# Kernel tuning notes

Measured on AMD Instinct MI355X. Metric: run time of the kernel, lower is better.

The kernel has to match this reference:

```python
import jax, jax.numpy as jnp
import numpy as np

N = 50000      # nodes
E = 800000     # top-down edges (before self-loops)
IN = 256       # in_dim
HID = 64       # hidden_dim
H = 4          # heads
SLOPE = 0.2    # PyG GATConv leaky_relu negative_slope


def setup_inputs() -> dict:
    key = jax.random.key(0)
    ks = jax.random.split(key, 12)
    g = lambda k, s, fan: jax.random.normal(k, s, dtype=jnp.float32) / np.float32(np.sqrt(fan))
    return {
        "x": jax.random.normal(ks[0], (N, IN), dtype=jnp.float32),
        "root_features": jax.random.normal(ks[1], (N, IN), dtype=jnp.float32),
        "edge_index": jax.random.randint(ks[2], (2, E), 0, N, dtype=jnp.int32),
        "W1": g(ks[3], (H * HID, IN), IN),
        "a_src1": g(ks[4], (H, HID), HID),
        "a_dst1": g(ks[5], (H, HID), HID),
        "b1": jnp.zeros((H * HID,), jnp.float32),
        "W2": g(ks[6], (H * HID, H * HID), H * HID),
        "a_src2": g(ks[7], (H, HID), HID),
        "a_dst2": g(ks[8], (H, HID), HID),
        "b2": jnp.zeros((HID,), jnp.float32),
        "Wr": g(ks[9], (HID, IN), IN),
        "br": jnp.zeros((HID,), jnp.float32),
    }


def gat_conv(h_in, src, dst, W, a_src, a_dst, bias, concat):
    """PyG GATConv (eval mode): gather -> attention logit -> segment softmax -> scatter."""
    h = (h_in @ W.T).reshape(-1, H, HID)                 # [N, H, C]
    alpha_s = jnp.einsum('nhc,hc->nh', h, a_src)         # [N, H]
    alpha_d = jnp.einsum('nhc,hc->nh', h, a_dst)
    logits = jax.nn.leaky_relu(alpha_s[src] + alpha_d[dst], SLOPE)   # [Etot, H]
    # numerically stable softmax over incoming edges of each dst node
    m = jax.ops.segment_max(logits, dst, num_segments=N)             # [N, H]
    e = jnp.exp(logits - m[dst])
    denom = jax.ops.segment_sum(e, dst, num_segments=N)              # [N, H]
    alpha = e / denom[dst]                                           # self-loops => denom > 0
    out = jax.ops.segment_sum(alpha[:, :, None] * h[src], dst, num_segments=N)  # [N, H, C]
    if concat:
        return out.reshape(-1, H * HID) + bias
    return out.mean(axis=1) + bias


def reference(x, root_features, edge_index, W1, a_src1, a_dst1, b1,
              W2, a_src2, a_dst2, b2, Wr, br):
    # PyG GATConv adds self-loops by default
    loops = jnp.arange(N, dtype=edge_index.dtype)
    src = jnp.concatenate([edge_index[0], loops])   # parents (message sources)
    dst = jnp.concatenate([edge_index[1], loops])   # children (aggregation targets)

    h = gat_conv(x, src, dst, W1, a_src1, a_dst1, b1, concat=True)   # [N, H*HID]
    h = jax.nn.relu(h)                                               # dropout = identity in eval
    h = gat_conv(h, src, dst, W2, a_src2, a_dst2, b2, concat=False)  # [N, HID]
    return h + root_features @ Wr.T + br
```

## Files before the change

kernel.cpp:

```cpp
#include <hip/hip_runtime.h>
#include <hip/hip_bf16.h>
#include <math.h>

#define NN   50000
#define EE   800000
#define ETOT (EE + NN)
#define KDIM 256
#define HEADS 4
#define HIDD 64
#define DCAP 64

typedef float  f32x4  __attribute__((ext_vector_type(4)));
typedef short  bf16x8 __attribute__((ext_vector_type(8)));

__device__ __forceinline__ float b2f(unsigned short u) {
    union { float f; unsigned int i; } v; v.i = (unsigned int)u << 16; return v.f;
}
__device__ __forceinline__ unsigned short f2b(float f) {
    union { float f; unsigned int i; } v; v.f = f;
    return (unsigned short)((v.i + 0x7fffu + ((v.i >> 16) & 1u)) >> 16);
}
__device__ __forceinline__ float lrelu(float x) { return x >= 0.f ? x : 0.2f * x; }

#define CASTB 144

__global__ __launch_bounds__(256) void prep_k(
    const float* __restrict__ W1, const float* __restrict__ W2,
    const float* __restrict__ Wr, unsigned short* __restrict__ wout)
{
    int i = (blockIdx.x * 256 + threadIdx.x) * 4;
    const float* src;
    int off;
    if (i < 65536)        { src = W1; off = 0; }
    else if (i < 131072)  { src = W2; off = 65536; }
    else                  { src = Wr; off = 131072; }
    float4 v = *reinterpret_cast<const float4*>(src + (i - off));
    ushort4 o;
    o.x = f2b(v.x); o.y = f2b(v.y); o.z = f2b(v.z); o.w = f2b(v.w);
    *reinterpret_cast<ushort4*>(wout + i) = o;
}

template<bool AF32, int NCT, bool ALPHA, bool OUTF32>
__device__ __forceinline__ void gemm_body(
    unsigned short (*__restrict__ Wl)[40], int bid,
    const void* __restrict__ Ain, const unsigned short* __restrict__ W,
    void* __restrict__ Cout, int Mrows,
    const float* __restrict__ av_src, const float* __restrict__ av_dst,
    float* __restrict__ AS, float* __restrict__ AD,
    const float* __restrict__ bias0, const float* __restrict__ bias1)
{
    constexpr int ROWS = NCT * 16;
    constexpr int KS   = 32;
    constexpr int NSL  = KDIM / KS;
    constexpr int NLD  = (ROWS * KS) / (256 * 8);

    const int t    = threadIdx.x;
    const int wid  = t >> 6;
    const int lane = t & 63;
    const int cl   = lane & 15;
    const int kg   = lane >> 4;
    const int m0   = (bid * 4 + wid) * 16;

    int arow = m0 + cl; if (arow >= Mrows) arow = Mrows - 1;

    bf16x8 stg[NLD];
    auto LOADSTG = [&](int s) {
        #pragma unroll
        for (int i = 0; i < NLD; i++) {
            int f = i * 256 + t;
            int c = f >> 2, kc = f & 3;
            stg[i] = *reinterpret_cast<const bf16x8*>(
                W + (size_t)c * KDIM + s * KS + kc * 8);
        }
    };
    auto WRITESTG = [&](int b) {
        #pragma unroll
        for (int i = 0; i < NLD; i++) {
            int f = i * 256 + t;
            int c = f >> 2, kc = f & 3;
            *reinterpret_cast<bf16x8*>(&Wl[b * ROWS + c][kc * 8]) = stg[i];
        }
    };
    auto LOADA = [&](int s) -> bf16x8 {
        if constexpr (AF32) {
            const float* ap = (const float*)Ain + (size_t)arow * KDIM + s * KS + kg * 8;
            float4 v0 = *reinterpret_cast<const float4*>(ap);
            float4 v1 = *reinterpret_cast<const float4*>(ap + 4);
            bf16x8 a;
            a[0] = (short)f2b(v0.x); a[1] = (short)f2b(v0.y);
            a[2] = (short)f2b(v0.z); a[3] = (short)f2b(v0.w);
            a[4] = (short)f2b(v1.x); a[5] = (short)f2b(v1.y);
            a[6] = (short)f2b(v1.z); a[7] = (short)f2b(v1.w);
            return a;
        } else {
            return *reinterpret_cast<const bf16x8*>(
                (const unsigned short*)Ain + (size_t)arow * KDIM + s * KS + kg * 8);
        }
    };

    f32x4 acc[NCT];
    #pragma unroll
    for (int ct = 0; ct < NCT; ct++) acc[ct] = (f32x4)(0.f);

    LOADSTG(0);
    WRITESTG(0);
    bf16x8 a_cur = LOADA(0);
    __syncthreads();

    int buf = 0;
    for (int s = 0; s < NSL; s++) {
        bf16x8 a_nxt;
        if (s + 1 < NSL) { LOADSTG(s + 1); a_nxt = LOADA(s + 1); }
        #pragma unroll
        for (int ct = 0; ct < NCT; ct++) {
            bf16x8 b = *reinterpret_cast<const bf16x8*>(&Wl[buf * ROWS + ct * 16 + cl][kg * 8]);
            acc[ct] = __builtin_amdgcn_mfma_f32_16x16x32_bf16(a_cur, b, acc[ct], 0, 0, 0);
        }
        if (s + 1 < NSL) {
            WRITESTG(buf ^ 1);
            __syncthreads();
            buf ^= 1;
            a_cur = a_nxt;
        }
    }

    if constexpr (OUTF32) {
        float* C = (float*)Cout;
        #pragma unroll
        for (int ct = 0; ct < NCT; ct++) {
            #pragma unroll
            for (int r = 0; r < 4; r++) {
                int n = m0 + kg * 4 + r;
                int c = ct * 16 + cl;
                if (n < Mrows)
                    C[(size_t)n * (NCT * 16) + c] = acc[ct][r] + bias0[c] + bias1[c];
            }
        }
    } else {
        unsigned short* C = (unsigned short*)Cout;
        #pragma unroll
        for (int ct = 0; ct < NCT; ct++) {
            #pragma unroll
            for (int r = 0; r < 4; r++) {
                int n = m0 + kg * 4 + r;
                if (n < Mrows)
                    C[(size_t)n * (NCT * 16) + ct * 16 + cl] = f2b(acc[ct][r]);
            }
        }
    }

    if constexpr (ALPHA) {
        float asr[NCT], adr[NCT];
        #pragma unroll
        for (int ct = 0; ct < NCT; ct++) {
            int c = ct * 16 + cl;
            asr[ct] = av_src[c];
            adr[ct] = av_dst[c];
        }
        #pragma unroll
        for (int r = 0; r < 4; r++) {
            int n = m0 + kg * 4 + r;
            f32x4 s4 = (f32x4)(0.f), d4 = (f32x4)(0.f);
            #pragma unroll
            for (int h = 0; h < 4; h++) {
                #pragma unroll
                for (int q = 0; q < 4; q++) {
                    s4[h] += acc[h * 4 + q][r] * asr[h * 4 + q];
                    d4[h] += acc[h * 4 + q][r] * adr[h * 4 + q];
                }
            }
            #pragma unroll
            for (int msk = 1; msk <= 8; msk <<= 1) {
                #pragma unroll
                for (int h = 0; h < 4; h++) {
                    s4[h] += __shfl_xor(s4[h], msk, 64);
                    d4[h] += __shfl_xor(d4[h], msk, 64);
                }
            }
            if (cl == 0 && n < Mrows) {
                *reinterpret_cast<float4*>(AS + (size_t)n * 4) =
                    make_float4(s4[0], s4[1], s4[2], s4[3]);
                *reinterpret_cast<float4*>(AD + (size_t)n * 4) =
                    make_float4(d4[0], d4[1], d4[2], d4[3]);
            }
        }
    }
}

#define MG   ((NN + 63) / 64)
#define FCH  576

__global__ __launch_bounds__(320) void mega1_k(
    const float* __restrict__ x, const unsigned short* __restrict__ w1b,
    unsigned short* __restrict__ Hb,
    const float* __restrict__ as1, const float* __restrict__ ad1,
    float* __restrict__ AS, float* __restrict__ AD,
    const float* __restrict__ root, const unsigned short* __restrict__ wrb,
    float* __restrict__ out, const float* __restrict__ br, const float* __restrict__ b2,
    const int* __restrict__ ei, int* __restrict__ deg, int* __restrict__ EDG)
{
    __shared__ unsigned short Wl[2 * 256][40];
    const int b = blockIdx.x;
    const int wid = threadIdx.x >> 6;

    if (wid < 4) {
        if (b < MG)
            gemm_body<true, 16, true, false>(Wl, b, x, w1b, Hb, NN,
                                             as1, ad1, AS, AD, nullptr, nullptr);
        else
            gemm_body<true, 4, false, true>(Wl, b - MG, root, wrb, out, NN,
                                            nullptr, nullptr, nullptr, nullptr, br, b2);
    } else {
        const int lane = threadIdx.x & 63;
        const int base = b * FCH;
        auto doEdge = [&](int e) {
            if (e < ETOT) {
                int src, dst;
                if (e < EE) { src = ei[e]; dst = ei[EE + e]; }
                else        { src = dst = e - EE; }
                int pos = atomicAdd(deg + dst, 1) & (DCAP - 1);
                EDG[(size_t)dst * DCAP + pos] = src;
            }
        };
        #pragma unroll
        for (int s = 0; s < 8; s++) {
            doEdge(base + s * 72 + lane);
            if (lane < 8) doEdge(base + s * 72 + 64 + lane);
            __syncthreads();
        }
    }
}

__global__ __launch_bounds__(256) void gemm2_k(
    const unsigned short* __restrict__ X2b, const unsigned short* __restrict__ w2b,
    unsigned short* __restrict__ Hb,
    const float* __restrict__ as2, const float* __restrict__ ad2,
    float* __restrict__ AS, float* __restrict__ AD)
{
    __shared__ unsigned short Wl[2 * 256][40];
    gemm_body<false, 16, true, false>(Wl, blockIdx.x, X2b, w2b, Hb, NN,
                                      as2, ad2, AS, AD, nullptr, nullptr);
}

template<int MODE>
__global__ __launch_bounds__(256) void gather_k(
    const int* __restrict__ deg, const int* __restrict__ EDG,
    const float* __restrict__ AS, const float* __restrict__ AD,
    const unsigned short* __restrict__ H, const float* __restrict__ bias,
    unsigned short* __restrict__ OUT, float* __restrict__ OUTF)
{
    __shared__ float wT[4][4][65];
    int wid  = threadIdx.x >> 6;
    int lane = threadIdx.x & 63;
    int n = blockIdx.x * 4 + wid;
    if (n >= NN) return;
    int head = lane >> 4;

    int cd = min(deg[n], DCAP);
    float4 ad4 = *reinterpret_cast<const float4*>(AD + (size_t)n * 4);

    int srcv = (lane < cd) ? EDG[(size_t)n * DCAP + lane] : 0;
    float4 w4 = make_float4(0.f, 0.f, 0.f, 0.f);
    if (lane < cd) {
        float4 s4 = *reinterpret_cast<const float4*>(AS + (size_t)srcv * 4);
        w4.x = __expf(lrelu(s4.x + ad4.x));
        w4.y = __expf(lrelu(s4.y + ad4.y));
        w4.z = __expf(lrelu(s4.z + ad4.z));
        w4.w = __expf(lrelu(s4.w + ad4.w));
    }
    wT[wid][0][lane] = w4.x;
    wT[wid][1][lane] = w4.y;
    wT[wid][2][lane] = w4.z;
    wT[wid][3][lane] = w4.w;

    float4 den4 = w4;
    #pragma unroll
    for (int msk = 1; msk <= 32; msk <<= 1) {
        den4.x += __shfl_xor(den4.x, msk, 64);
        den4.y += __shfl_xor(den4.y, msk, 64);
        den4.z += __shfl_xor(den4.z, msk, 64);
        den4.w += __shfl_xor(den4.w, msk, 64);
    }
    float den = head == 0 ? den4.x : head == 1 ? den4.y : head == 2 ? den4.z : den4.w;
    float inv = 1.f / den;

    float a0 = 0.f, a1 = 0.f, a2 = 0.f, a3 = 0.f;
    float c0 = 0.f, c1 = 0.f, c2 = 0.f, c3 = 0.f;
    const unsigned short* hp = H + lane * 4;

    int j = 0;
    for (; j + 4 <= cd; j += 4) {
        int   sA = __builtin_amdgcn_readlane(srcv, j);
        int   sB = __builtin_amdgcn_readlane(srcv, j + 1);
        int   sC = __builtin_amdgcn_readlane(srcv, j + 2);
        int   sD = __builtin_amdgcn_readlane(srcv, j + 3);
        float wA = wT[wid][head][j];
        float wB = wT[wid][head][j + 1];
        float wC = wT[wid][head][j + 2];
        float wD = wT[wid][head][j + 3];
        ushort4 hA = *reinterpret_cast<const ushort4*>(hp + (size_t)sA * 256);
        ushort4 hB = *reinterpret_cast<const ushort4*>(hp + (size_t)sB * 256);
        ushort4 hC = *reinterpret_cast<const ushort4*>(hp + (size_t)sC * 256);
        ushort4 hD = *reinterpret_cast<const ushort4*>(hp + (size_t)sD * 256);
        a0 += wA * b2f(hA.x); a1 += wA * b2f(hA.y);
        a2 += wA * b2f(hA.z); a3 += wA * b2f(hA.w);
        c0 += wB * b2f(hB.x); c1 += wB * b2f(hB.y);
        c2 += wB * b2f(hB.z); c3 += wB * b2f(hB.w);
        a0 += wC * b2f(hC.x); a1 += wC * b2f(hC.y);
        a2 += wC * b2f(hC.z); a3 += wC * b2f(hC.w);
        c0 += wD * b2f(hD.x); c1 += wD * b2f(hD.y);
        c2 += wD * b2f(hD.z); c3 += wD * b2f(hD.w);
    }
    for (; j < cd; j++) {
        int   sA = __builtin_amdgcn_readlane(srcv, j);
        float wA = wT[wid][head][j];
        ushort4 hA = *reinterpret_cast<const ushort4*>(hp + (size_t)sA * 256);
        a0 += wA * b2f(hA.x); a1 += wA * b2f(hA.y);
        a2 += wA * b2f(hA.z); a3 += wA * b2f(hA.w);
    }
    a0 += c0; a1 += c1; a2 += c2; a3 += c3;

    if (MODE == 1) {
        float4 bv = *reinterpret_cast<const float4*>(bias + lane * 4);
        ushort4 o;
        o.x = f2b(fmaxf(a0 * inv + bv.x, 0.f));
        o.y = f2b(fmaxf(a1 * inv + bv.y, 0.f));
        o.z = f2b(fmaxf(a2 * inv + bv.z, 0.f));
        o.w = f2b(fmaxf(a3 * inv + bv.w, 0.f));
        *reinterpret_cast<ushort4*>(OUT + (size_t)n * 256 + lane * 4) = o;
    } else {
        float v0 = a0 * inv, v1 = a1 * inv, v2 = a2 * inv, v3 = a3 * inv;
        #pragma unroll
        for (int msk = 16; msk <= 32; msk <<= 1) {
            v0 += __shfl_xor(v0, msk, 64);
            v1 += __shfl_xor(v1, msk, 64);
            v2 += __shfl_xor(v2, msk, 64);
            v3 += __shfl_xor(v3, msk, 64);
        }
        if (lane < 16) {
            float4* o = reinterpret_cast<float4*>(OUTF + (size_t)n * 64 + lane * 4);
            float4 cur = *o;
            cur.x += 0.25f * v0;
            cur.y += 0.25f * v1;
            cur.z += 0.25f * v2;
            cur.w += 0.25f * v3;
            *o = cur;
        }
    }
}

extern "C" void kernel_launch(void* const* d_in, const int* in_sizes, int n_in,
                              void* d_out, int out_size, void* d_ws, size_t ws_size,
                              hipStream_t stream) {
    const float* x    = (const float*)d_in[0];
    const float* root = (const float*)d_in[1];
    const int*   ei   = (const int*)  d_in[2];
    const float* W1   = (const float*)d_in[3];
    const float* as1  = (const float*)d_in[4];
    const float* ad1  = (const float*)d_in[5];
    const float* b1   = (const float*)d_in[6];
    const float* W2   = (const float*)d_in[7];
    const float* as2  = (const float*)d_in[8];
    const float* ad2  = (const float*)d_in[9];
    const float* b2   = (const float*)d_in[10];
    const float* Wr   = (const float*)d_in[11];
    const float* br   = (const float*)d_in[12];
    float* out = (float*)d_out;

    unsigned short* Hb  = (unsigned short*)d_ws;
    unsigned short* X2b = Hb  + (size_t)NN * 256;
    unsigned short* w1b = X2b + (size_t)NN * 256;
    unsigned short* w2b = w1b + 65536;
    unsigned short* wrb = w2b + 65536;
    float* AS  = (float*)(wrb + 16384);
    float* AD  = AS + (size_t)NN * 4;
    int*   deg = (int*)(AD + (size_t)NN * 4);
    int*   EDG = deg + NN;

    const int wgrid = (NN + 3) / 4;

    hipMemsetAsync(deg, 0, NN * sizeof(int), stream);
    prep_k<<<CASTB, 256, 0, stream>>>(W1, W2, Wr, w1b);

    mega1_k<<<2 * MG, 320, 0, stream>>>(x, w1b, Hb, as1, ad1, AS, AD,
                                        root, wrb, out, br, b2,
                                        ei, deg, EDG);
    gather_k<1><<<wgrid, 256, 0, stream>>>(deg, EDG, AS, AD, Hb, b1, X2b, nullptr);

    gemm2_k<<<MG, 256, 0, stream>>>(X2b, w2b, Hb, as2, ad2, AS, AD);
    gather_k<2><<<wgrid, 256, 0, stream>>>(deg, EDG, AS, AD, Hb, nullptr, nullptr, out);
}
```

Before: 237.2 us.

## Replace global-atomic edge bucketing with two-pass shared-memory binning by destination

Edge bucketing is split out of the fused GEMM kernel into two passes. The first pass bins edges by destination block of 512 nodes in shared memory, then flushes each bin to a global partition buffer. The second pass builds the per-node adjacency lists using only shared-memory atomics. This removes scattered global atomics on the degree array and drops the fused warp-specialised kernel, but adds two launches, an extra round trip of edge data through global memory, and a fixed per-bin capacity (PCAP) that could overflow on skewed graphs.

```diff
diff --git a/kernel.cpp b/kernel.cpp
--- a/kernel.cpp
+++ b/kernel.cpp
@@ -38,6 +38,75 @@
     ushort4 o;
     o.x = f2b(v.x); o.y = f2b(v.y); o.z = f2b(v.z); o.w = f2b(v.w);
     *reinterpret_cast<ushort4*>(wout + i) = o;
+}
+
+#define NCH   2048
+#define ACH   ((ETOT + NCH - 1) / NCH)
+#define CB    98
+#define BCAP  56
+#define PCAP  9728
+
+__global__ __launch_bounds__(256) void binA_k(
+    const int* __restrict__ ei, int* __restrict__ PCNT, uint2* __restrict__ PART)
+{
+    __shared__ uint2 bins[CB][BCAP];
+    __shared__ int   bcnt[CB];
+    const int t = threadIdx.x;
+    for (int i = t; i < CB; i += 256) bcnt[i] = 0;
+    __syncthreads();
+
+    const int base = blockIdx.x * NCH;
+    #pragma unroll
+    for (int i = 0; i < NCH / 256; i++) {
+        int e = base + i * 256 + t;
+        if (e < ETOT) {
+            int src, dst;
+            if (e < EE) { src = ei[e]; dst = ei[EE + e]; }
+            else        { src = dst = e - EE; }
+            int b = dst >> 9;
+            int p = atomicAdd(&bcnt[b], 1);
+            if (p < BCAP) {
+                bins[b][p] = make_uint2((unsigned)src, (unsigned)dst);
+            } else {
+                int gp = atomicAdd(&PCNT[b], 1);
+                PART[(size_t)b * PCAP + gp] = make_uint2((unsigned)src, (unsigned)dst);
+            }
+        }
+    }
+    __syncthreads();
+
+    const int wid = t >> 6, lane = t & 63;
+    for (int b = wid; b < CB; b += 4) {
+        int cnt = min(bcnt[b], BCAP);
+        if (cnt == 0) continue;
+        int rbase = 0;
+        if (lane == 0) rbase = atomicAdd(&PCNT[b], cnt);
+        rbase = __builtin_amdgcn_readfirstlane(rbase);
+        for (int j = lane; j < cnt; j += 64)
+            PART[(size_t)b * PCAP + rbase + j] = bins[b][j];
+    }
+}
+
+__global__ __launch_bounds__(512) void binB_k(
+    const int* __restrict__ PCNT, const uint2* __restrict__ PART,
+    int* __restrict__ deg, int* __restrict__ EDG)
+{
+    __shared__ int ldeg[512];
+    const int t = threadIdx.x;
+    const int b = blockIdx.x;
+    ldeg[t] = 0;
+    __syncthreads();
+
+    const int nbase = b << 9;
+    const int cnt = PCNT[b];
+    for (int i = t; i < cnt; i += 512) {
+        uint2 ed = PART[(size_t)b * PCAP + i];
+        int p = atomicAdd(&ldeg[(int)ed.y - nbase], 1) & (DCAP - 1);
+        EDG[(size_t)ed.y * DCAP + p] = (int)ed.x;
+    }
+    __syncthreads();
+    int n = nbase + t;
+    if (n < NN) deg[n] = ldeg[t];
 }
 
 template<bool AF32, int NCT, bool ALPHA, bool OUTF32>
@@ -187,48 +256,23 @@
     }
 }
 
-#define MG   ((NN + 63) / 64)
-#define FCH  576
-
-__global__ __launch_bounds__(320) void mega1_k(
+#define MG ((NN + 63) / 64)
+
+__global__ __launch_bounds__(256) void gemm1root_k(
     const float* __restrict__ x, const unsigned short* __restrict__ w1b,
     unsigned short* __restrict__ Hb,
     const float* __restrict__ as1, const float* __restrict__ ad1,
     float* __restrict__ AS, float* __restrict__ AD,
     const float* __restrict__ root, const unsigned short* __restrict__ wrb,
-    float* __restrict__ out, const float* __restrict__ br, const float* __restrict__ b2,
-    const int* __restrict__ ei, int* __restrict__ deg, int* __restrict__ EDG)
+    float* __restrict__ out, const float* __restrict__ br, const float* __restrict__ b2)
 {
     __shared__ unsigned short Wl[2 * 256][40];
-    const int b = blockIdx.x;
-    const int wid = threadIdx.x >> 6;
-
-    if (wid < 4) {
-        if (b < MG)
-            gemm_body<true, 16, true, false>(Wl, b, x, w1b, Hb, NN,
-                                             as1, ad1, AS, AD, nullptr, nullptr);
-        else
-            gemm_body<true, 4, false, true>(Wl, b - MG, root, wrb, out, NN,
-                                            nullptr, nullptr, nullptr, nullptr, br, b2);
-    } else {
-        const int lane = threadIdx.x & 63;
-        const int base = b * FCH;
-        auto doEdge = [&](int e) {
-            if (e < ETOT) {
-                int src, dst;
-                if (e < EE) { src = ei[e]; dst = ei[EE + e]; }
-                else        { src = dst = e - EE; }
-                int pos = atomicAdd(deg + dst, 1) & (DCAP - 1);
-                EDG[(size_t)dst * DCAP + pos] = src;
-            }
-        };
-        #pragma unroll
-        for (int s = 0; s < 8; s++) {
-            doEdge(base + s * 72 + lane);
-            if (lane < 8) doEdge(base + s * 72 + 64 + lane);
-            __syncthreads();
-        }
-    }
+    if (blockIdx.x < MG)
+        gemm_body<true, 16, true, false>(Wl, blockIdx.x, x, w1b, Hb, NN,
+                                         as1, ad1, AS, AD, nullptr, nullptr);
+    else
+        gemm_body<true, 4, false, true>(Wl, blockIdx.x - MG, root, wrb, out, NN,
+                                        nullptr, nullptr, nullptr, nullptr, br, b2);
 }
 
 __global__ __launch_bounds__(256) void gemm2_k(
@@ -376,15 +420,19 @@
     float* AD  = AS + (size_t)NN * 4;
     int*   deg = (int*)(AD + (size_t)NN * 4);
     int*   EDG = deg + NN;
+    int*   PCNT = EDG + (size_t)NN * DCAP;
+    uint2* PART = (uint2*)(PCNT + 128);
 
     const int wgrid = (NN + 3) / 4;
 
-    hipMemsetAsync(deg, 0, NN * sizeof(int), stream);
+    hipMemsetAsync(PCNT, 0, CB * sizeof(int), stream);
     prep_k<<<CASTB, 256, 0, stream>>>(W1, W2, Wr, w1b);
 
-    mega1_k<<<2 * MG, 320, 0, stream>>>(x, w1b, Hb, as1, ad1, AS, AD,
-                                        root, wrb, out, br, b2,
-                                        ei, deg, EDG);
+    binA_k<<<ACH, 256, 0, stream>>>(ei, PCNT, PART);
+    binB_k<<<CB, 512, 0, stream>>>(PCNT, PART, deg, EDG);
+
+    gemm1root_k<<<2 * MG, 256, 0, stream>>>(x, w1b, Hb, as1, ad1, AS, AD,
+                                            root, wrb, out, br, b2);
     gather_k<1><<<wgrid, 256, 0, stream>>>(deg, EDG, AS, AD, Hb, b1, X2b, nullptr);
 
     gemm2_k<<<MG, 256, 0, stream>>>(X2b, w2b, Hb, as2, ad2, AS, AD);
```

New measurement: 499.6 us. 2.11x slower.
